# Performance work log

Measured on AMD Instinct MI355X. Metric: run time of the kernel, lower is better.

## Reference

```python
import jax, jax.numpy as jnp
import numpy as np

BM = 192  # query block size (kernel hard-coded to BM=192)


def setup_inputs() -> dict:
    key = jax.random.key(0)
    k1, k2, k3 = jax.random.split(key, 3)
    B, H, S, D = 1, 12, 3840, 128
    q = jax.random.normal(k1, (B, H, S, D), dtype=jnp.float32)
    k = jax.random.normal(k2, (B, H, S, D), dtype=jnp.float32)
    v = jax.random.normal(k3, (B, H, S, D), dtype=jnp.float32)
    topk = 1024
    return {"q": q, "k": k, "v": v, "topk": topk}


def reference(q, k, v, topk):
    # Chipmunk SparseDiffAttn core pipeline:
    # 1) dense_colsum_attn: dense attention whose probs are column-summed per
    #    192-query block to produce block scores bs [B,H,QG,S]
    # 2) topk index selection per query group (mask -> indices)
    # 3) csp_attn: block-sparse attention where each 192-query group attends
    #    only to its selected top-k keys
    B, H, S, D = q.shape
    QG = S // BM
    scale = 1.0 / np.sqrt(D)

    # --- dense colsum attention (scoring pass) ---
    scores = jnp.einsum('bhqd,bhkd->bhqk', q, k) * scale      # [B,H,S,S]
    probs = jax.nn.softmax(scores, axis=-1)                   # [B,H,S,S]
    # column-sum of attention probs within each 192-query block
    bs = probs.reshape(B, H, QG, BM, S).sum(axis=-2)          # [B,H,QG,S]

    # --- topk mask -> per-group key indices ---
    _, inds = jax.lax.top_k(bs, topk)                         # [B,H,QG,TK] int32

    # --- block-sparse gather attention (csp_attn) ---
    # gather selected keys/values per query group
    gather = jax.vmap(jax.vmap(lambda kv, idx: kv[idx]))      # over B, H
    kg = gather(k, inds)                                      # [B,H,QG,TK,D]
    vg = gather(v, inds)                                      # [B,H,QG,TK,D]
    qg = q.reshape(B, H, QG, BM, D)                           # [B,H,QG,BM,D]

    s2 = jnp.einsum('bhgqd,bhgkd->bhgqk', qg, kg) * scale     # [B,H,QG,BM,TK]
    p2 = jax.nn.softmax(s2, axis=-1)
    o = jnp.einsum('bhgqk,bhgkd->bhgqd', p2, vg)              # [B,H,QG,BM,D]
    return o.reshape(B, H, S, D)
```

## Files before the change

kernel.cpp:

```cpp
#include <hip/hip_runtime.h>
#include <math.h>


#define HH 12
#define SS 3840
#define DD 128
#define QGn 20
#define TKn 1024
#define NROWS (HH * QGn)
#define HS (HH * SS)
#define NT 60
#define TCH 3072
#define SCALE_D 0.08838834764831845
#define SCALE_F 0.08838834764831845f

typedef short short8 __attribute__((ext_vector_type(8)));
typedef float f32x4 __attribute__((ext_vector_type(4)));

#define MFMA(a, b, c) __builtin_amdgcn_mfma_f32_16x16x32_bf16(a, b, c, 0, 0, 0)
#define MFMA_B16(c, a, b) \
  c = __builtin_amdgcn_mfma_f32_16x16x32_bf16(a, b, c, 0, 0, 0)

typedef __attribute__((address_space(3))) unsigned int lds_u32;
typedef const __attribute__((address_space(1))) unsigned int glb_u32;

__device__ __forceinline__ unsigned short bf_rne(float x) {
  unsigned u = __float_as_uint(x);
  u = (u + 0x7fffu + ((u >> 16) & 1u)) >> 16;
  return (unsigned short)u;
}
__device__ __forceinline__ float bf_f(unsigned short b) {
  return __uint_as_float(((unsigned)b) << 16);
}
__device__ __forceinline__ void split3(float f, unsigned short& a,
                                       unsigned short& b, unsigned short& c) {
  a = bf_rne(f);
  float r = f - bf_f(a);
  b = bf_rne(r);
  r = r - bf_f(b);
  c = bf_rne(r);
}
__device__ __forceinline__ void split2(float f, unsigned short& a,
                                       unsigned short& b) {
  a = bf_rne(f);
  float r = f - bf_f(a);
  b = bf_rne(r);
}
__device__ __forceinline__ short8 ldfrag(const unsigned short* base, int chunk) {
  return *(const short8*)&base[(size_t)chunk * 8];
}

__global__ __launch_bounds__(1024) void presplit_kernel(
    const float* __restrict__ q, const float* __restrict__ k,
    unsigned short* __restrict__ qsplit, unsigned short* __restrict__ ksplit) {
  const int t = threadIdx.x;
  const int lane = t & 63;
  const int u = t >> 6;
  const int kc = u & 3, kt = u >> 2;
  const int ln = lane & 15, quad = lane >> 4;
  const int c = blockIdx.x;
  const int h = blockIdx.y;
  const float* src = blockIdx.z ? k : q;
  unsigned short* dst = blockIdx.z ? ksplit : qsplit;

  const float* p =
      &src[(size_t)(h * SS + c * 64 + kt * 16 + ln) * DD + kc * 32 + quad * 8];
  float b8[8];
  *(float4*)&b8[0] = *(const float4*)&p[0];
  *(float4*)&b8[4] = *(const float4*)&p[4];
  unsigned short f0[8], f1[8], f2[8];
#pragma unroll
  for (int e = 0; e < 8; ++e) split3(b8[e], f0[e], f1[e], f2[e]);
  size_t base =
      ((size_t)(h * NT + c) * TCH + ((kt * 4 + kc) * 3) * 64 + lane) * 8;
  *(ushort4*)&dst[base + 0] = *(ushort4*)&f0[0];
  *(ushort4*)&dst[base + 4] = *(ushort4*)&f0[4];
  *(ushort4*)&dst[base + 512] = *(ushort4*)&f1[0];
  *(ushort4*)&dst[base + 516] = *(ushort4*)&f1[4];
  *(ushort4*)&dst[base + 1024] = *(ushort4*)&f2[0];
  *(ushort4*)&dst[base + 1028] = *(ushort4*)&f2[4];
}

__global__ __launch_bounds__(256) void stats_mfma(
    const unsigned short* __restrict__ qsplit,
    const unsigned short* __restrict__ ksplit,
    double* __restrict__ lpart) {
  __shared__ __align__(16) unsigned short Bs[3][6144];
  const int t = threadIdx.x;
  const int w = t >> 6;
  const int lane = t & 63;
  const int ln = lane & 15;
  const int quad = lane >> 4;
  const int h = blockIdx.y;
  const int nq = blockIdx.z;
  const int q0 = blockIdx.x * 128 + w * 32;
  const int tq = blockIdx.x * 2 + (w >> 1);
  const int ktA = (w & 1) * 2;

  short8 A[2][4][3];
  {
    const unsigned short* qb = &qsplit[(size_t)(h * NT + tq) * TCH * 8];
#pragma unroll
    for (int s = 0; s < 2; ++s)
#pragma unroll
      for (int kc = 0; kc < 4; ++kc)
#pragma unroll
        for (int cm = 0; cm < 3; ++cm)
          A[s][kc][cm] =
              ldfrag(qb, (((ktA + s) * 4 + kc) * 3 + cm) * 64 + lane);
  }

  double racc[2][4];
#pragma unroll
  for (int s = 0; s < 2; ++s)
#pragma unroll
    for (int r = 0; r < 4; ++r) racc[s][r] = 0.0;

  const unsigned short* kq = &ksplit[(size_t)(h * NT + nq * 15) * TCH * 8];

#define STG_S(slot, j)                                                     \
  do {                                                                     \
    const unsigned short* src_ = kq + (size_t)(j) * 6144 + t * 8;          \
    __builtin_amdgcn_global_load_lds((glb_u32*)(src_),                     \
        (lds_u32*)&Bs[slot][w * 512], 16, 0, 0);                           \
    __builtin_amdgcn_global_load_lds((glb_u32*)(src_ + 2048),              \
        (lds_u32*)&Bs[slot][2048 + w * 512], 16, 0, 0);                    \
    __builtin_amdgcn_global_load_lds((glb_u32*)(src_ + 4096),              \
        (lds_u32*)&Bs[slot][4096 + w * 512], 16, 0, 0);                    \
  } while (0)

  const f32x4 z = {0.f, 0.f, 0.f, 0.f};
  f32x4 C[2][3];

  STG_S(0, 0);

  int cur = 0;
#pragma unroll 1
  for (int j = 0; j < 60; ++j) {
    __builtin_amdgcn_sched_barrier(0);
    if (j < 59) {
      const int nxt = (cur == 2) ? 0 : cur + 1;
      STG_S(nxt, j + 1);
      asm volatile("s_waitcnt vmcnt(3)" ::: "memory");
    } else {
      asm volatile("s_waitcnt vmcnt(0)" ::: "memory");
    }
    __builtin_amdgcn_s_barrier();
    __builtin_amdgcn_sched_barrier(0);
    __builtin_amdgcn_s_setprio(1);
    if (j > 0) {
#pragma unroll
      for (int s = 0; s < 2; ++s)
#pragma unroll
        for (int r = 0; r < 4; ++r) {
          float sv = (C[s][0][r] + C[s][1][r]) + C[s][2][r];
          racc[s][r] += (double)__expf(sv * SCALE_F);
        }
    }
    const unsigned short* Bp = &Bs[cur][0];
#pragma unroll
    for (int kc = 0; kc < 4; ++kc) {
      short8 B0 = *(const short8*)&Bp[(kc * 3 + 0) * 512 + lane * 8];
      short8 B1 = *(const short8*)&Bp[(kc * 3 + 1) * 512 + lane * 8];
      short8 B2 = *(const short8*)&Bp[(kc * 3 + 2) * 512 + lane * 8];
#pragma unroll
      for (int s = 0; s < 2; ++s) {
        if (kc == 0) {
          C[s][0] = MFMA(A[s][0][0], B0, z);
          C[s][1] = MFMA(A[s][0][0], B1, z);
          C[s][1] = MFMA(A[s][0][1], B0, C[s][1]);
          C[s][0] = MFMA(A[s][0][1], B1, C[s][0]);
          C[s][2] = MFMA(A[s][0][2], B0, z);
          C[s][2] = MFMA(A[s][0][0], B2, C[s][2]);
        } else {
          MFMA_B16(C[s][0], A[s][kc][0], B0);
          MFMA_B16(C[s][1], A[s][kc][0], B1);
          MFMA_B16(C[s][1], A[s][kc][1], B0);
          MFMA_B16(C[s][0], A[s][kc][1], B1);
          MFMA_B16(C[s][2], A[s][kc][2], B0);
          MFMA_B16(C[s][2], A[s][kc][0], B2);
        }
      }
    }
    __builtin_amdgcn_s_setprio(0);
    cur = (cur == 2) ? 0 : cur + 1;
  }
#undef STG_S

#pragma unroll
  for (int s = 0; s < 2; ++s)
#pragma unroll
    for (int r = 0; r < 4; ++r) {
      float sv = (C[s][0][r] + C[s][1][r]) + C[s][2][r];
      racc[s][r] += (double)__expf(sv * SCALE_F);
    }

#pragma unroll
  for (int s = 0; s < 2; ++s)
#pragma unroll
    for (int r = 0; r < 4; ++r) {
      double v = racc[s][r];
      v += __shfl_xor(v, 1);
      v += __shfl_xor(v, 2);
      v += __shfl_xor(v, 4);
      v += __shfl_xor(v, 8);
      if (ln == 0)
        lpart[(size_t)nq * HS + h * SS + q0 + s * 16 + quad * 4 + r] = v;
    }
}

__global__ __launch_bounds__(256) void colsum_mfma(
    const unsigned short* __restrict__ qsplit,
    const unsigned short* __restrict__ ksplit,
    const double* __restrict__ lpart, double* __restrict__ bs) {
  __shared__ double rls[192];
  __shared__ __align__(16) unsigned short As[3][6144];
  const int t = threadIdx.x;
  const int w = t >> 6;
  const int lane = t & 63;
  const int ln = lane & 15;
  const int quad = lane >> 4;
  const int h = blockIdx.z, g = blockIdx.y;
  const int k0 = blockIdx.x * 128 + w * 32;
  const int tk = blockIdx.x * 2 + (w >> 1);
  const int ktB = (w & 1) * 2;

  short8 Bk[2][4][3];
  {
    const unsigned short* kb = &ksplit[(size_t)(h * NT + tk) * TCH * 8];
#pragma unroll
    for (int s = 0; s < 2; ++s)
#pragma unroll
      for (int kc = 0; kc < 4; ++kc)
#pragma unroll
        for (int cm = 0; cm < 3; ++cm)
          Bk[s][kc][cm] =
              ldfrag(kb, (((ktB + s) * 4 + kc) * 3 + cm) * 64 + lane);
  }

  if (t < 192) {
    size_t qi = h * SS + g * 192 + t;
    rls[t] = 1.0 / (lpart[qi] + lpart[HS + qi] + lpart[2 * (size_t)HS + qi] +
                    lpart[3 * (size_t)HS + qi]);
  }
  __syncthreads();

  double cacc[2] = {0.0, 0.0};

  const unsigned short* qg = &qsplit[(size_t)(h * NT + g * 3) * TCH * 8];

#define STG_C(slot, j)                                                     \
  do {                                                                     \
    const unsigned short* src_ = qg + (size_t)(j) * 6144 + t * 8;          \
    __builtin_amdgcn_global_load_lds((glb_u32*)(src_),                     \
        (lds_u32*)&As[slot][w * 512], 16, 0, 0);                           \
    __builtin_amdgcn_global_load_lds((glb_u32*)(src_ + 2048),              \
        (lds_u32*)&As[slot][2048 + w * 512], 16, 0, 0);                    \
    __builtin_amdgcn_global_load_lds((glb_u32*)(src_ + 4096),              \
        (lds_u32*)&As[slot][4096 + w * 512], 16, 0, 0);                    \
  } while (0)

  const f32x4 z = {0.f, 0.f, 0.f, 0.f};
  f32x4 C[2][3];

  STG_C(0, 0);

  int cur = 0;
#pragma unroll 1
  for (int j = 0; j < 12; ++j) {
    __builtin_amdgcn_sched_barrier(0);
    if (j < 11) {
      const int nxt = (cur == 2) ? 0 : cur + 1;
      STG_C(nxt, j + 1);
      asm volatile("s_waitcnt vmcnt(3)" ::: "memory");
    } else {
      asm volatile("s_waitcnt vmcnt(0)" ::: "memory");
    }
    __builtin_amdgcn_s_barrier();
    __builtin_amdgcn_sched_barrier(0);
    __builtin_amdgcn_s_setprio(1);
    if (j > 0) {
      const int qprev = (j - 1) * 16;
#pragma unroll
      for (int s = 0; s < 2; ++s)
#pragma unroll
        for (int r = 0; r < 4; ++r) {
          float p = __expf(((C[s][0][r] + C[s][1][r]) + C[s][2][r]) * SCALE_F);
          cacc[s] += (double)p * rls[qprev + quad * 4 + r];
        }
    }
    const unsigned short* Ap = &As[cur][0];
#pragma unroll
    for (int kc = 0; kc < 4; ++kc) {
      short8 A0 = *(const short8*)&Ap[(kc * 3 + 0) * 512 + lane * 8];
      short8 A1 = *(const short8*)&Ap[(kc * 3 + 1) * 512 + lane * 8];
      short8 A2 = *(const short8*)&Ap[(kc * 3 + 2) * 512 + lane * 8];
#pragma unroll
      for (int s = 0; s < 2; ++s) {
        if (kc == 0) {
          C[s][0] = MFMA(A0, Bk[s][0][0], z);
          C[s][1] = MFMA(A1, Bk[s][0][0], z);
          C[s][1] = MFMA(A0, Bk[s][0][1], C[s][1]);
          C[s][0] = MFMA(A1, Bk[s][0][1], C[s][0]);
          C[s][2] = MFMA(A2, Bk[s][0][0], z);
          C[s][2] = MFMA(A0, Bk[s][0][2], C[s][2]);
        } else {
          MFMA_B16(C[s][0], A0, Bk[s][kc][0]);
          MFMA_B16(C[s][1], A1, Bk[s][kc][0]);
          MFMA_B16(C[s][1], A0, Bk[s][kc][1]);
          MFMA_B16(C[s][0], A1, Bk[s][kc][1]);
          MFMA_B16(C[s][2], A2, Bk[s][kc][0]);
          MFMA_B16(C[s][2], A0, Bk[s][kc][2]);
        }
      }
    }
    __builtin_amdgcn_s_setprio(0);
    cur = (cur == 2) ? 0 : cur + 1;
  }
#undef STG_C

#pragma unroll
  for (int s = 0; s < 2; ++s)
#pragma unroll
    for (int r = 0; r < 4; ++r) {
      float p = __expf(((C[s][0][r] + C[s][1][r]) + C[s][2][r]) * SCALE_F);
      cacc[s] += (double)p * rls[176 + quad * 4 + r];
    }

#pragma unroll
  for (int s = 0; s < 2; ++s) {
    double v = cacc[s];
    v += __shfl_xor(v, 16);
    v += __shfl_xor(v, 32);
    if (quad == 0)
      bs[(size_t)(h * QGn + g) * SS + k0 + s * 16 + ln] = v;
  }
}

__global__ __launch_bounds__(256) void topk3_kernel(
    const double* __restrict__ bs, int* __restrict__ inds,
    double* __restrict__ bnd_val, int* __restrict__ bnd_idx) {
  __shared__ unsigned long long u[SS];
  __shared__ int hist[256];
  __shared__ int sfx[256];
  __shared__ int s_bin, s_r;
  __shared__ int c_gt, c_eq;
  __shared__ unsigned long long rv[256];
  __shared__ int ri[256];
  const int t = threadIdx.x;
  const int row = blockIdx.x;
  const double* vals = bs + (size_t)row * SS;

  for (int i = t; i < SS; i += 256)
    u[i] = (unsigned long long)__double_as_longlong(vals[i]);

  unsigned long long pref = 0ull;
  int r = TKn;
  for (int shift = 56; shift >= 0; shift -= 8) {
    hist[t] = 0;
    __syncthreads();
    unsigned long long himask =
        (shift == 56) ? 0ull : (0xFFFFFFFFFFFFFFFFull << (shift + 8));
    for (int i = t; i < SS; i += 256) {
      unsigned long long uv = u[i];
      if ((uv & himask) == (pref & himask))
        atomicAdd(&hist[(int)((uv >> shift) & 255)], 1);
    }
    __syncthreads();
    sfx[t] = hist[t];
    __syncthreads();
#pragma unroll
    for (int off = 1; off < 256; off <<= 1) {
      int v = (t + off < 256) ? sfx[t + off] : 0;
      __syncthreads();
      sfx[t] += v;
      __syncthreads();
    }
    {
      int St = sfx[t];
      int Sn = (t == 255) ? 0 : sfx[t + 1];
      if (St >= r && Sn < r) {
        s_bin = t;
        s_r = r - Sn;
      }
    }
    if (t == 0) {
      c_gt = 0;
      c_eq = 0;
    }
    __syncthreads();
    pref |= ((unsigned long long)s_bin) << shift;
    r = s_r;
    __syncthreads();
  }
  const int G = TKn - r;
  int* out = inds + (size_t)row * TKn;
  unsigned long long mb = 0ull;
  int mbi = -1;
  for (int i = t; i < SS; i += 256) {
    unsigned long long uv = u[i];
    if (uv > pref) {
      int p = atomicAdd(&c_gt, 1);
      out[p] = i;
    } else if (uv == pref) {
      int e = atomicAdd(&c_eq, 1);
      if (e < r) out[G + e] = i;
      if (e == r - 1) bnd_idx[row * 2 + 0] = i;
    } else if (uv > mb) {
      mb = uv;
      mbi = i;
    }
  }
  rv[t] = mb;
  ri[t] = mbi;
  __syncthreads();
  for (int s2 = 128; s2 > 0; s2 >>= 1) {
    if (t < s2 && rv[t + s2] > rv[t]) {
      rv[t] = rv[t + s2];
      ri[t] = ri[t + s2];
    }
    __syncthreads();
  }
  if (t == 0) {
    bnd_val[row * 2 + 0] = __longlong_as_double((long long)pref);
    bnd_val[row * 2 + 1] = __longlong_as_double((long long)rv[0]);
    bnd_idx[row * 2 + 1] = ri[0];
  }
}

__global__ __launch_bounds__(256) void argmin_kernel(
    const double* __restrict__ bnd_val, const int* __restrict__ bnd_idx,
    int* __restrict__ rsel) {
  __shared__ double gmin[256];
  __shared__ int grow[256];
  const int t = threadIdx.x;
  double g = 1e300;
  int r = -1;
  if (t < NROWS) {
    g = bnd_val[t * 2 + 0] - bnd_val[t * 2 + 1];
    r = t;
  }
  gmin[t] = g;
  grow[t] = r;
  __syncthreads();
  for (int s2 = 128; s2 > 0; s2 >>= 1) {
    if (t < s2 && gmin[t + s2] < gmin[t]) {
      gmin[t] = gmin[t + s2];
      grow[t] = grow[t + s2];
    }
    __syncthreads();
  }
  if (t == 0) {
    int rr = grow[0];
    rsel[0] = rr;
    rsel[1] = bnd_idx[rr * 2 + 0];
    rsel[2] = bnd_idx[rr * 2 + 1];
  }
}

__global__ __launch_bounds__(256) void exact_rl_kernel(
    const float* __restrict__ q, const float* __restrict__ k,
    const int* __restrict__ rsel, double* __restrict__ rl_exact) {
  __shared__ double qd[DD];
  __shared__ double red[256];
  const int t = threadIdx.x;
  const int row = rsel[0];
  const int h = row / QGn, g = row % QGn;
  const float* qp = &q[(size_t)(h * SS + g * 192 + blockIdx.x) * DD];
  if (t < DD) qd[t] = (double)qp[t];
  __syncthreads();
  double l = 0.0;
  for (int kk = t; kk < SS; kk += 256) {
    const float* kp = &k[(size_t)(h * SS + kk) * DD];
    double s = 0.0;
#pragma unroll 4
    for (int d = 0; d < DD; d += 4) {
      float4 kv = *(const float4*)&kp[d];
      s += qd[d] * (double)kv.x + qd[d + 1] * (double)kv.y +
           qd[d + 2] * (double)kv.z + qd[d + 3] * (double)kv.w;
    }
    l += exp(s * SCALE_D);
  }
  red[t] = l;
  __syncthreads();
  for (int s2 = 128; s2 > 0; s2 >>= 1) {
    if (t < s2) red[t] += red[t + s2];
    __syncthreads();
  }
  if (t == 0) rl_exact[blockIdx.x] = 1.0 / red[0];
}

__global__ __launch_bounds__(256) void exact_pair_kernel(
    const float* __restrict__ q, const float* __restrict__ k,
    const int* __restrict__ rsel, const double* __restrict__ rl_exact,
    int* __restrict__ inds) {
  __shared__ double redX[256], redY[256];
  const int t = threadIdx.x;
  const int row = rsel[0], kept = rsel[1], drop = rsel[2];
  const int h = row / QGn, g = row % QGn;
  double px = 0.0, py = 0.0;
  if (t < 192) {
    const float* qp = &q[(size_t)(h * SS + g * 192 + t) * DD];
    const float* kx = &k[(size_t)(h * SS + kept) * DD];
    const float* ky = &k[(size_t)(h * SS + drop) * DD];
    double sx = 0.0, sy = 0.0;
#pragma unroll 4
    for (int d = 0; d < DD; ++d) {
      double qv = (double)qp[d];
      sx += qv * (double)kx[d];
      sy += qv * (double)ky[d];
    }
    double rv = rl_exact[t];
    px = exp(sx * SCALE_D) * rv;
    py = exp(sy * SCALE_D) * rv;
  }
  redX[t] = px;
  redY[t] = py;
  __syncthreads();
  for (int s2 = 128; s2 > 0; s2 >>= 1) {
    if (t < s2) { redX[t] += redX[t + s2]; redY[t] += redY[t + s2]; }
    __syncthreads();
  }
  if (t == 0)
    inds[(size_t)row * TKn + (TKn - 1)] = (redX[0] <= redY[0]) ? kept : drop;
}

__global__ __launch_bounds__(256, 3) void sparse_attn_mfma(
    const float* __restrict__ q, const float* __restrict__ k,
    const float* __restrict__ v, const int* __restrict__ inds,
    float* __restrict__ out) {
  __shared__ unsigned short ksm[2][32][136];
  __shared__ unsigned short vsm[2][128][40];
  __shared__ unsigned short pbuf[4][2][16][40];
  const int t = threadIdx.x;
  const int w = t >> 6;
  const int lane = t & 63;
  const int ln = lane & 15;
  const int quad = lane >> 4;
  const int h = blockIdx.z, g = blockIdx.y;
  const int qbase = g * 192 + blockIdx.x * 64;
  const int* ip = &inds[(size_t)(h * QGn + g) * TKn];

  short8 A[4][2];
  {
    const float* qp = &q[(size_t)(h * SS + qbase + w * 16 + ln) * DD + quad * 8];
#pragma unroll
    for (int kc = 0; kc < 4; ++kc) {
      float b8[8];
      *(float4*)&b8[0] = *(const float4*)&qp[kc * 32];
      *(float4*)&b8[4] = *(const float4*)&qp[kc * 32 + 4];
      short8 f0, f1;
#pragma unroll
      for (int e = 0; e < 8; ++e) {
        unsigned short x0, x1;
        split2(b8[e], x0, x1);
        f0[e] = (short)x0; f1[e] = (short)x1;
      }
      A[kc][0] = f0; A[kc][1] = f1;
    }
  }

  f32x4 O[8];
#pragma unroll
  for (int dt = 0; dt < 8; ++dt) O[dt] = (f32x4){0.f, 0.f, 0.f, 0.f};
  float lacc[4] = {0.f, 0.f, 0.f, 0.f};

  const int kk = t >> 3;
  const int sub = t & 7;

  float4 rk[4], rv4[4];
  {
    int gk = ip[kk];
    const float* kp = &k[(size_t)(h * SS + gk) * DD + sub * 16];
    const float* vp = &v[(size_t)(h * SS + gk) * DD + sub * 16];
#pragma unroll
    for (int e4 = 0; e4 < 4; ++e4) {
      rk[e4] = *(const float4*)&kp[e4 * 4];
      rv4[e4] = *(const float4*)&vp[e4 * 4];
    }
  }

  for (int kt = 0; kt < TKn; kt += 32) {
    __syncthreads();
#pragma unroll
    for (int e4 = 0; e4 < 4; ++e4) {
      float4 kv = rk[e4];
      ushort4 k0, k1;
      split2(kv.x, k0.x, k1.x);
      split2(kv.y, k0.y, k1.y);
      split2(kv.z, k0.z, k1.z);
      split2(kv.w, k0.w, k1.w);
      *(ushort4*)&ksm[0][kk][sub * 16 + e4 * 4] = k0;
      *(ushort4*)&ksm[1][kk][sub * 16 + e4 * 4] = k1;
      float4 vv = rv4[e4];
      ushort4 v0, v1;
      split2(vv.x, v0.x, v1.x);
      split2(vv.y, v0.y, v1.y);
      split2(vv.z, v0.z, v1.z);
      split2(vv.w, v0.w, v1.w);
      int d0 = sub * 16 + e4 * 4;
      vsm[0][d0 + 0][kk] = v0.x; vsm[1][d0 + 0][kk] = v1.x;
      vsm[0][d0 + 1][kk] = v0.y; vsm[1][d0 + 1][kk] = v1.y;
      vsm[0][d0 + 2][kk] = v0.z; vsm[1][d0 + 2][kk] = v1.z;
      vsm[0][d0 + 3][kk] = v0.w; vsm[1][d0 + 3][kk] = v1.w;
    }
    __syncthreads();

    if (kt + 32 < TKn) {
      int gk = ip[kt + 32 + kk];
      const float* kp = &k[(size_t)(h * SS + gk) * DD + sub * 16];
      const float* vp = &v[(size_t)(h * SS + gk) * DD + sub * 16];
#pragma unroll
      for (int e4 = 0; e4 < 4; ++e4) {
        rk[e4] = *(const float4*)&kp[e4 * 4];
        rv4[e4] = *(const float4*)&vp[e4 * 4];
      }
    }

#pragma unroll
    for (int s = 0; s < 2; ++s) {
      f32x4 C0 = {0.f, 0.f, 0.f, 0.f};
      f32x4 C1 = C0;
      __builtin_amdgcn_s_setprio(1);
#pragma unroll
      for (int kc = 0; kc < 4; ++kc) {
        short8 B0 = *(const short8*)&ksm[0][s * 16 + ln][kc * 32 + quad * 8];
        short8 B1 = *(const short8*)&ksm[1][s * 16 + ln][kc * 32 + quad * 8];
        MFMA_B16(C0, A[kc][0], B0);
        MFMA_B16(C1, A[kc][1], B0);
        MFMA_B16(C1, A[kc][0], B1);
      }
      __builtin_amdgcn_s_setprio(0);
#pragma unroll
      for (int r = 0; r < 4; ++r) {
        float pv = __expf((C0[r] + C1[r]) * SCALE_F);
        lacc[r] += pv;
        unsigned short p0, p1;
        split2(pv, p0, p1);
        pbuf[w][0][quad * 4 + r][s * 16 + ln] = p0;
        pbuf[w][1][quad * 4 + r][s * 16 + ln] = p1;
      }
    }
    short8 P0 = *(const short8*)&pbuf[w][0][ln][quad * 8];
    short8 P1 = *(const short8*)&pbuf[w][1][ln][quad * 8];
    __builtin_amdgcn_s_setprio(1);
#pragma unroll
    for (int dt = 0; dt < 8; ++dt) {
      short8 V0 = *(const short8*)&vsm[0][dt * 16 + ln][quad * 8];
      short8 V1 = *(const short8*)&vsm[1][dt * 16 + ln][quad * 8];
      MFMA_B16(O[dt], P0, V0);
      MFMA_B16(O[dt], P1, V0);
      MFMA_B16(O[dt], P0, V1);
    }
    __builtin_amdgcn_s_setprio(0);
  }

#pragma unroll
  for (int r = 0; r < 4; ++r) {
    float l = lacc[r];
    l += __shfl_xor(l, 1);
    l += __shfl_xor(l, 2);
    l += __shfl_xor(l, 4);
    l += __shfl_xor(l, 8);
    float rl = 1.f / l;
    float* op = &out[(size_t)(h * SS + qbase + w * 16 + quad * 4 + r) * DD];
#pragma unroll
    for (int dt = 0; dt < 8; ++dt) op[dt * 16 + ln] = O[dt][r] * rl;
  }
}

extern "C" void kernel_launch(void* const* d_in, const int* in_sizes, int n_in,
                              void* d_out, int out_size, void* d_ws, size_t ws_size,
                              hipStream_t stream) {
  const float* q = (const float*)d_in[0];
  const float* k = (const float*)d_in[1];
  const float* v = (const float*)d_in[2];
  float* out = (float*)d_out;

  const size_t SPLIT_ELEMS = (size_t)HH * NT * TCH * 8;
  unsigned short* qsplit = (unsigned short*)d_ws;
  unsigned short* ksplit = qsplit + SPLIT_ELEMS;
  double* lpart = (double*)(ksplit + SPLIT_ELEMS);
  double* bs = lpart + 4 * (size_t)HS;
  int* inds = (int*)(bs + (size_t)HH * QGn * SS);
  double* bnd_val = (double*)(inds + (size_t)NROWS * TKn);
  int* bnd_idx = (int*)(bnd_val + (size_t)NROWS * 2);
  int* rsel = bnd_idx + NROWS * 2;
  double* rl_exact = (double*)(rsel + 4);

  presplit_kernel<<<dim3(NT, HH, 2), 1024, 0, stream>>>(q, k, qsplit, ksplit);
  stats_mfma<<<dim3(SS / 128, HH, 4), 256, 0, stream>>>(qsplit, ksplit, lpart);
  colsum_mfma<<<dim3(SS / 128, QGn, HH), 256, 0, stream>>>(qsplit, ksplit, lpart, bs);
  topk3_kernel<<<dim3(NROWS), 256, 0, stream>>>(bs, inds, bnd_val, bnd_idx);
  argmin_kernel<<<dim3(1), 256, 0, stream>>>(bnd_val, bnd_idx, rsel);
  exact_rl_kernel<<<dim3(192), 256, 0, stream>>>(q, k, rsel, rl_exact);
  exact_pair_kernel<<<dim3(1), 256, 0, stream>>>(q, k, rsel, rl_exact, inds);
  sparse_attn_mfma<<<dim3(3, QGn, HH), 256, 0, stream>>>(q, k, v, inds, out);
}
```

Baseline: 801.0 us.

## Load presplit bf16 K directly into LDS via global_load_lds in sparse attention

New measurement: 781.5 us. -2.4%, faster.

```diff
diff --git a/kernel.cpp b/kernel.cpp
--- a/kernel.cpp
+++ b/kernel.cpp
@@ -526,10 +526,10 @@
 }
 
 __global__ __launch_bounds__(256, 3) void sparse_attn_mfma(
-    const float* __restrict__ q, const float* __restrict__ k,
-    const float* __restrict__ v, const int* __restrict__ inds,
+    const float* __restrict__ q, const float* __restrict__ v,
+    const int* __restrict__ inds, const unsigned short* __restrict__ ksplit,
     float* __restrict__ out) {
-  __shared__ unsigned short ksm[2][32][136];
+  __shared__ __align__(16) unsigned short ksmN[16 * 512];
   __shared__ unsigned short vsm[2][128][40];
   __shared__ unsigned short pbuf[4][2][16][40];
   const int t = threadIdx.x;
@@ -540,6 +540,7 @@
   const int h = blockIdx.z, g = blockIdx.y;
   const int qbase = g * 192 + blockIdx.x * 64;
   const int* ip = &inds[(size_t)(h * QGn + g) * TKn];
+  const unsigned short* kbh = &ksplit[(size_t)(h * NT) * (TCH * 8)];
 
   short8 A[4][2];
   {
@@ -567,31 +568,43 @@
 
   const int kk = t >> 3;
   const int sub = t & 7;
-
-  float4 rk[4], rv4[4];
+  const int sW = w >> 1;
+  const int c0 = w * 4;
+
+  int gkA = ip[sW * 16 + ln];
+  float4 rv4[4];
   {
-    int gk = ip[kk];
-    const float* kp = &k[(size_t)(h * SS + gk) * DD + sub * 16];
-    const float* vp = &v[(size_t)(h * SS + gk) * DD + sub * 16];
+    int gkV = ip[kk];
+    const float* vp = &v[(size_t)(h * SS + gkV) * DD + sub * 16];
+#pragma unroll
+    for (int e4 = 0; e4 < 4; ++e4) rv4[e4] = *(const float4*)&vp[e4 * 4];
+  }
+
+  for (int kt = 0; kt < TKn; kt += 32) {
+    __builtin_amdgcn_s_barrier();
+    __builtin_amdgcn_sched_barrier(0);
+    const bool more = (kt + 32 < TKn);
+    int gkVn = 0, gkAn = 0;
+    if (more) {
+      gkVn = ip[kt + 32 + kk];
+      gkAn = ip[kt + 32 + sW * 16 + ln];
+    }
+    {
+      const unsigned short* rowp = kbh + (size_t)(gkA >> 6) * (TCH * 8) +
+                                   ((gkA & 15) + 16 * quad) * 8;
+      const int ktile = (gkA >> 4) & 3;
+#pragma unroll
+      for (int i = 0; i < 4; ++i) {
+        const int c16 = c0 + i;
+        const int kc = (c16 >> 1) & 3;
+        const int cm = c16 & 1;
+        __builtin_amdgcn_global_load_lds(
+            (glb_u32*)(rowp + ((ktile * 4 + kc) * 3 + cm) * 512),
+            (lds_u32*)&ksmN[c16 * 512], 16, 0, 0);
+      }
+    }
 #pragma unroll
     for (int e4 = 0; e4 < 4; ++e4) {
-      rk[e4] = *(const float4*)&kp[e4 * 4];
-      rv4[e4] = *(const float4*)&vp[e4 * 4];
-    }
-  }
-
-  for (int kt = 0; kt < TKn; kt += 32) {
-    __syncthreads();
-#pragma unroll
-    for (int e4 = 0; e4 < 4; ++e4) {
-      float4 kv = rk[e4];
-      ushort4 k0, k1;
-      split2(kv.x, k0.x, k1.x);
-      split2(kv.y, k0.y, k1.y);
-      split2(kv.z, k0.z, k1.z);
-      split2(kv.w, k0.w, k1.w);
-      *(ushort4*)&ksm[0][kk][sub * 16 + e4 * 4] = k0;
-      *(ushort4*)&ksm[1][kk][sub * 16 + e4 * 4] = k1;
       float4 vv = rv4[e4];
       ushort4 v0, v1;
       split2(vv.x, v0.x, v1.x);
@@ -604,18 +617,17 @@
       vsm[0][d0 + 2][kk] = v0.z; vsm[1][d0 + 2][kk] = v1.z;
       vsm[0][d0 + 3][kk] = v0.w; vsm[1][d0 + 3][kk] = v1.w;
     }
-    __syncthreads();
-
-    if (kt + 32 < TKn) {
-      int gk = ip[kt + 32 + kk];
-      const float* kp = &k[(size_t)(h * SS + gk) * DD + sub * 16];
-      const float* vp = &v[(size_t)(h * SS + gk) * DD + sub * 16];
-#pragma unroll
-      for (int e4 = 0; e4 < 4; ++e4) {
-        rk[e4] = *(const float4*)&kp[e4 * 4];
-        rv4[e4] = *(const float4*)&vp[e4 * 4];
-      }
-    }
+    if (more) {
+      const float* vp = &v[(size_t)(h * SS + gkVn) * DD + sub * 16];
+#pragma unroll
+      for (int e4 = 0; e4 < 4; ++e4) rv4[e4] = *(const float4*)&vp[e4 * 4];
+      asm volatile("s_waitcnt vmcnt(4) lgkmcnt(0)" ::: "memory");
+      gkA = gkAn;
+    } else {
+      asm volatile("s_waitcnt vmcnt(0) lgkmcnt(0)" ::: "memory");
+    }
+    __builtin_amdgcn_s_barrier();
+    __builtin_amdgcn_sched_barrier(0);
 
 #pragma unroll
     for (int s = 0; s < 2; ++s) {
@@ -624,8 +636,8 @@
       __builtin_amdgcn_s_setprio(1);
 #pragma unroll
       for (int kc = 0; kc < 4; ++kc) {
-        short8 B0 = *(const short8*)&ksm[0][s * 16 + ln][kc * 32 + quad * 8];
-        short8 B1 = *(const short8*)&ksm[1][s * 16 + ln][kc * 32 + quad * 8];
+        short8 B0 = *(const short8*)&ksmN[(s * 8 + kc * 2 + 0) * 512 + lane * 8];
+        short8 B1 = *(const short8*)&ksmN[(s * 8 + kc * 2 + 1) * 512 + lane * 8];
         MFMA_B16(C0, A[kc][0], B0);
         MFMA_B16(C1, A[kc][1], B0);
         MFMA_B16(C1, A[kc][0], B1);
@@ -695,5 +707,5 @@
   argmin_kernel<<<dim3(1), 256, 0, stream>>>(bnd_val, bnd_idx, rsel);
   exact_rl_kernel<<<dim3(192), 256, 0, stream>>>(q, k, rsel, rl_exact);
   exact_pair_kernel<<<dim3(1), 256, 0, stream>>>(q, k, rsel, rl_exact, inds);
-  sparse_attn_mfma<<<dim3(3, QGn, HH), 256, 0, stream>>>(q, k, v, inds, out);
-}
+  sparse_attn_mfma<<<dim3(3, QGn, HH), 256, 0, stream>>>(q, v, inds, ksplit, out);
+}
```
